# Optimization experiments

Hardware: AMD Instinct MI355X
Metric: run time of the kernel (lower is better)

## Reference

```python
import math
import jax, jax.numpy as jnp
import numpy as np

HIDDEN = 1024
HEADS = 16
HEAD_DIM = HIDDEN // HEADS  # 64
SEQ = 4096
PATCH = 4064  # num rotated (patch) tokens; last PATCH positions get RoPE
EPS = 1e-6


def setup_inputs() -> dict:
    key = jax.random.key(0)
    ks = jax.random.split(key, 8)
    return {
        "x": jax.random.normal(ks[0], (1, SEQ, HIDDEN), dtype=jnp.float32),
        "rope_cos": jax.random.uniform(ks[1], (PATCH, HEAD_DIM // 2), dtype=jnp.float32),
        "rope_sin": jax.random.uniform(ks[2], (PATCH, HEAD_DIM // 2), dtype=jnp.float32),
        "wq": jax.random.normal(ks[3], (HIDDEN, HIDDEN), dtype=jnp.float32) / math.sqrt(HIDDEN),
        "wk": jax.random.normal(ks[4], (HIDDEN, HIDDEN), dtype=jnp.float32) / math.sqrt(HIDDEN),
        "wv": jax.random.normal(ks[5], (HIDDEN, HIDDEN), dtype=jnp.float32) / math.sqrt(HIDDEN),
        "wo": jax.random.normal(ks[6], (HIDDEN, HIDDEN), dtype=jnp.float32) / math.sqrt(HIDDEN),
        "q_norm_w": jnp.ones((HEAD_DIM,), dtype=jnp.float32),
        "k_norm_w": jnp.ones((HEAD_DIM,), dtype=jnp.float32),
    }


def _rms_norm(t, w):
    # RMSNorm over the last (head_dim) axis
    return t * jax.lax.rsqrt(jnp.mean(t * t, axis=-1, keepdims=True) + EPS) * w


def _apply_rope(t, cos, sin):
    # t: [b, s, h, d]; rotate only the last PATCH positions, pairwise complex mul
    b, s, h, d = t.shape
    P = cos.shape[0]
    tail = t[:, s - P:].reshape(b, P, h, d // 2, 2)
    x0, x1 = tail[..., 0], tail[..., 1]
    c = cos[None, :, None, :]
    sn = sin[None, :, None, :]
    rot = jnp.stack([x0 * c - x1 * sn, x0 * sn + x1 * c], axis=-1).reshape(b, P, h, d)
    return jnp.concatenate([t[:, : s - P], rot], axis=1)


def reference(x, rope_cos, rope_sin, wq, wk, wv, wo, q_norm_w, k_norm_w):
    b, s, _ = x.shape
    q = (x @ wq.T).reshape(b, s, HEADS, HEAD_DIM)
    k = (x @ wk.T).reshape(b, s, HEADS, HEAD_DIM)
    v = (x @ wv.T).reshape(b, s, HEADS, HEAD_DIM)
    q = _rms_norm(q, q_norm_w)
    k = _rms_norm(k, k_norm_w)
    q = _apply_rope(q, rope_cos, rope_sin)
    k = _apply_rope(k, rope_cos, rope_sin)
    q = q / math.sqrt(HEAD_DIM)
    scores = jnp.einsum('bqhd,bkhd->bhqk', q, k)
    attn = jax.nn.softmax(scores.astype(jnp.float32), axis=-1)
    out = jnp.einsum('bhqk,bkhd->bqhd', attn, v).reshape(b, s, HIDDEN)
    return out @ wo.T
```

## Files before the change

kernel.cpp:

```cpp
#include <hip/hip_runtime.h>
#include <hip/hip_bf16.h>
#include <stdint.h>

#define HIDDEN 1024
#define HEADS 16
#define HEAD_DIM 64
#define SEQ 4096
#define PATCH 4064
#define SKIP 32

typedef __attribute__((ext_vector_type(8))) short bf16x8;
typedef __attribute__((ext_vector_type(4))) float f32x4;
typedef __attribute__((ext_vector_type(2))) float f32x2;
typedef __attribute__((ext_vector_type(16))) float f32x16;

__device__ __forceinline__ float b2f(unsigned short u){
  union{uint32_t i; float f;} c; c.i = ((uint32_t)u)<<16; return c.f;
}
__device__ __forceinline__ unsigned short f2b(float f){
  union{float f; uint32_t i;} c; c.f=f;
  uint32_t r = c.i + 0x7fffu + ((c.i>>16)&1u);
  return (unsigned short)(r>>16);
}
__device__ __forceinline__ uint32_t cvtpk(float a, float b){
  uint32_t r;
  asm("v_cvt_pk_bf16_f32 %0, %1, %2" : "=v"(r) : "v"(a), "v"(b));
  return r;
}

#define GLD16(gp, lp) __builtin_amdgcn_global_load_lds( \
    (const __attribute__((address_space(1))) void*)(gp), \
    (__attribute__((address_space(3))) void*)(lp), 16, 0, 0)

__global__ __launch_bounds__(256) void convert_all(
    const float* __restrict__ x,  const float* __restrict__ wq,
    const float* __restrict__ wk, const float* __restrict__ wv,
    const float* __restrict__ wo,
    unsigned short* __restrict__ xb,  unsigned short* __restrict__ wqb,
    unsigned short* __restrict__ wkb, unsigned short* __restrict__ wvb,
    unsigned short* __restrict__ wob)
{
  size_t u = (size_t)blockIdx.x*256 + threadIdx.x;
  size_t e = u*8;
  const float* src; unsigned short* dst; size_t off;
  if      (e < 4194304ull) { src=x;  dst=xb;  off=e;            }
  else if (e < 5242880ull) { src=wq; dst=wqb; off=e-4194304ull; }
  else if (e < 6291456ull) { src=wk; dst=wkb; off=e-5242880ull; }
  else if (e < 7340032ull) { src=wv; dst=wvb; off=e-6291456ull; }
  else                     { src=wo; dst=wob; off=e-7340032ull; }
  float4 v0 = *(const float4*)(src+off);
  float4 v1 = *(const float4*)(src+off+4);
  union { bf16x8 v; unsigned short h[8]; } o;
  o.h[0]=f2b(v0.x); o.h[1]=f2b(v0.y); o.h[2]=f2b(v0.z); o.h[3]=f2b(v0.w);
  o.h[4]=f2b(v1.x); o.h[5]=f2b(v1.y); o.h[6]=f2b(v1.z); o.h[7]=f2b(v1.w);
  *(bf16x8*)(dst+off) = o.v;
}

template<int MODE>
__global__ __launch_bounds__(256) void gemm_bt(
    const unsigned short* __restrict__ A,
    const unsigned short* __restrict__ B0,
    const unsigned short* __restrict__ B1,
    const unsigned short* __restrict__ B2,
    float* __restrict__ Cf,
    unsigned short* __restrict__ qout, unsigned short* __restrict__ kout,
    unsigned short* __restrict__ vout,
    const float* __restrict__ rc, const float* __restrict__ rs,
    const float* __restrict__ qw, const float* __restrict__ kw,
    int M, int Nper, int K)
{
  __shared__ unsigned short smem[16384];
  const int tid = threadIdx.x;
  const int w = tid>>6, l = tid&63;
  const int wm = w>>1, wn = w&1;
  const int g = l>>4, lr = l&15;
  const int bm = blockIdx.x;
  int bn = blockIdx.y;
  const int tilesPer = Nper >> 7;
  const int sel = bn / tilesPer;
  bn -= sel*tilesPer;
  const unsigned short* Bsel = (sel==0) ? B0 : ((sel==1) ? B1 : B2);

  const int off0 = w*1024 + l*16;
  const int r0 = off0>>6, c0 = (off0&63)>>1;
  const int off1 = off0 + 4096;
  const int r1 = off1>>6, c1 = (off1&63)>>1;

  const unsigned short* Ab = A    + (size_t)(bm*128)*K;
  const unsigned short* Bb = Bsel + (size_t)(bn*128)*K;

#define STG(db, kt) do { \
    GLD16(Ab + (size_t)r0*K + (kt) + c0, (char*)smem + (db) + off0); \
    GLD16(Ab + (size_t)r1*K + (kt) + c1, (char*)smem + (db) + off1); \
    GLD16(Bb + (size_t)r0*K + (kt) + c0, (char*)smem + (db) + 8192 + off0); \
    GLD16(Bb + (size_t)r1*K + (kt) + c1, (char*)smem + (db) + 8192 + off1); } while(0)

  f32x4 zero = {0.f,0.f,0.f,0.f};
  f32x4 acc[4][4];
  #pragma unroll
  for (int m=0;m<4;m++)
    #pragma unroll
    for (int n=0;n<4;n++) acc[m][n]=zero;

  const int nkt = K >> 5;
  STG(0, 0);
  for (int t = 0; t < nkt; ++t) {
    __syncthreads();
    const int db = (t&1)<<14;
    if (t+1 < nkt) STG(db^16384, (t+1)*32);
    bf16x8 a[4], b[4];
    #pragma unroll
    for (int m=0;m<4;m++)
      a[m] = *(const bf16x8*)((char*)smem + db + (wm*64 + m*16 + lr)*64 + g*16);
    #pragma unroll
    for (int n=0;n<4;n++)
      b[n] = *(const bf16x8*)((char*)smem + db + 8192 + (wn*64 + n*16 + lr)*64 + g*16);
    #pragma unroll
    for (int m=0;m<4;m++)
      #pragma unroll
      for (int n=0;n<4;n++)
        acc[m][n] = __builtin_amdgcn_mfma_f32_16x16x32_bf16(a[m], b[n], acc[m][n], 0,0,0);
  }
#undef STG

  if constexpr (MODE == 0) {
    #pragma unroll
    for (int m=0;m<4;m++){
      const int row = bm*128 + wm*64 + m*16 + g*4;
      #pragma unroll
      for (int n=0;n<4;n++){
        const int col = bn*128 + wn*64 + n*16 + lr;
        #pragma unroll
        for (int r=0;r<4;r++)
          Cf[(size_t)(row+r)*Nper + col] = acc[m][n][r];
      }
    }
  } else {
    if (sel <= 1) {
      const float* nw = (sel==0) ? qw : kw;
      unsigned short* dst = (sel==0) ? qout : kout;
      const float scl = (sel==0) ? 0.18033688011112042f : 1.0f;
      float wl[4];
      #pragma unroll
      for (int n=0;n<4;n++) wl[n] = nw[n*16+lr];
      const int hglob = bn*2 + wn;
      #pragma unroll
      for (int m=0;m<4;m++){
        const int rowb = bm*128 + wm*64 + m*16 + g*4;
        float rn[4];
        #pragma unroll
        for (int r=0;r<4;r++){
          float ss = 0.f;
          #pragma unroll
          for (int n=0;n<4;n++) ss += acc[m][n][r]*acc[m][n][r];
          ss += __shfl_xor(ss,1); ss += __shfl_xor(ss,2);
          ss += __shfl_xor(ss,4); ss += __shfl_xor(ss,8);
          rn[r] = rsqrtf(ss*(1.f/64.f) + 1e-6f);
        }
        #pragma unroll
        for (int r=0;r<4;r++){
          const int row = rowb + r;
          const int p = row - SKIP;
          #pragma unroll
          for (int n=0;n<4;n++){
            float v = acc[m][n][r]*rn[r]*wl[n];
            float c = 1.f, sn = 0.f;
            if (p >= 0){
              const int d2 = (n*16+lr)>>1;
              c  = rc[p*(HEAD_DIM/2) + d2];
              sn = rs[p*(HEAD_DIM/2) + d2];
            }
            const float partner = __shfl_xor(v, 1);
            const float o2 = (lr&1) ? (partner*sn + v*c) : (v*c - partner*sn);
            dst[(size_t)row*HIDDEN + hglob*64 + n*16 + lr] = f2b(o2*scl);
          }
        }
      }
    } else {
      #pragma unroll
      for (int m=0;m<4;m++){
        const int row = bm*128 + wm*64 + m*16 + g*4;
        #pragma unroll
        for (int n=0;n<4;n++){
          const int col = bn*128 + wn*64 + n*16 + lr;
          #pragma unroll
          for (int r=0;r<4;r++)
            vout[(size_t)(row+r)*HIDDEN + col] = f2b(acc[m][n][r]);
        }
      }
    }
  }
}

__global__ __launch_bounds__(256) void transpose_v(
    const unsigned short* __restrict__ v, unsigned short* __restrict__ vt)
{
  __shared__ unsigned short t[64*72];
  const int h = blockIdx.y;
  const int s0 = blockIdx.x * 64;
  const int tid = threadIdx.x;
  #pragma unroll
  for (int i=0;i<2;i++){
    const int e = tid + i*256;
    const int r = e>>3, cc = (e&7)*8;
    *(bf16x8*)&t[r*72+cc] = *(const bf16x8*)(v + (size_t)(s0+r)*HIDDEN + h*HEAD_DIM + cc);
  }
  __syncthreads();
  #pragma unroll
  for (int i=0;i<2;i++){
    const int e = tid + i*256;
    const int d = e>>3, sc = (e&7)*8;
    union { bf16x8 v8; unsigned short h8[8]; } o;
    #pragma unroll
    for (int j=0;j<8;j++){
      const int x  = sc + j;
      const int px = (x & ~12) | ((x&4)<<1) | ((x&8)>>1);
      o.h8[j] = t[px*72 + d];
    }
    *(bf16x8*)(vt + (size_t)(h*HEAD_DIM + d)*SEQ + s0 + sc) = o.v8;
  }
}

__device__ __forceinline__ void softmax_pack(f32x16 (&st)[2], f32x2 &lacc, bf16x8 (&pf)[4]){
  float pv[32];
  #pragma unroll
  for (int i=0;i<16;i++){
    pv[i]    = __builtin_amdgcn_exp2f(st[0][i]);
    pv[16+i] = __builtin_amdgcn_exp2f(st[1][i]);
  }
  #pragma unroll
  for (int i=0;i<8;i++){
    f32x2 a; a.x = pv[2*i];    a.y = pv[2*i+1];    lacc += a;
    f32x2 b; b.x = pv[16+2*i]; b.y = pv[16+2*i+1]; lacc += b;
  }
  #pragma unroll
  for (int t2=0; t2<2; t2++)
    #pragma unroll
    for (int e=0; e<2; e++){
      union { uint32_t u4[4]; bf16x8 v8; } pu;
      #pragma unroll
      for (int u=0; u<4; u++)
        pu.u4[u] = cvtpk(pv[t2*16+e*8+2*u], pv[t2*16+e*8+2*u+1]);
      pf[2*t2+e] = pu.v8;
    }
}

__global__ __launch_bounds__(256, 2) void attn_kernel(
    const unsigned short* __restrict__ q, const unsigned short* __restrict__ k,
    const unsigned short* __restrict__ vt, unsigned short* __restrict__ po,
    float* __restrict__ lbuf)
{
  __shared__ unsigned short smem[32768];
  const int fid = blockIdx.x + 16*(blockIdx.y + 16*blockIdx.z);
  const int h    = (fid&7)*2 + ((fid>>3)&1);
  const int rem  = fid>>4;
  const int q0   = (rem&15)*256;
  const int half = rem>>4;
  const int tid = threadIdx.x;
  const int w = tid>>6, l = tid&63;
  const int hi = l>>5, lo = l&31;
  const int NT = SEQ/128/2;
  const int tbase = half * NT;

  int kcol[4], vcol[4], vrow[4];
  #pragma unroll
  for (int i=0;i<4;i++){
    const int c = tid + i*256;
    const int rk = c>>3;
    kcol[i] = ((c&7)*16) ^ ((rk&7)<<4);
    const int rv = c>>4;
    vrow[i] = rv;
    vcol[i] = (((c&7)*16) ^ ((rv&7)<<4)) + ((c>>3)&1)*128;
  }
  const unsigned short* kPtr[4]; const unsigned short* vPtr[4];
  #pragma unroll
  for (int i=0;i<4;i++){
    kPtr[i] = k  + (size_t)((tid + i*256)>>3)*HIDDEN + h*HEAD_DIM + (kcol[i]>>1);
    vPtr[i] = vt + ((size_t)(h*HEAD_DIM + vrow[i]))*SEQ + (vcol[i]>>1);
  }

#define STAGE(b, kOffE, vOffE) do { \
    GLD16(kPtr[0] + (kOffE), (char*)smem + (b)*32768 + (tid      )*16); \
    GLD16(kPtr[1] + (kOffE), (char*)smem + (b)*32768 + (tid+ 256 )*16); \
    GLD16(kPtr[2] + (kOffE), (char*)smem + (b)*32768 + (tid+ 512 )*16); \
    GLD16(kPtr[3] + (kOffE), (char*)smem + (b)*32768 + (tid+ 768 )*16); \
    GLD16(vPtr[0] + (vOffE), (char*)smem + (b)*32768 + 16384 + (tid      )*16); \
    GLD16(vPtr[1] + (vOffE), (char*)smem + (b)*32768 + 16384 + (tid+ 256 )*16); \
    GLD16(vPtr[2] + (vOffE), (char*)smem + (b)*32768 + 16384 + (tid+ 512 )*16); \
    GLD16(vPtr[3] + (vOffE), (char*)smem + (b)*32768 + 16384 + (tid+ 768 )*16); \
  } while(0)

  const int swz = (lo&7)<<4;
  int colo[4];
  #pragma unroll
  for (int ks=0; ks<4; ks++) colo[ks] = ((2*ks+hi)*16) ^ swz;

  bf16x8 qf0[4], qf1[4];
  {
    const unsigned short* qp = q + (size_t)(q0 + w*64 + lo)*HIDDEN + h*HEAD_DIM;
    #pragma unroll
    for (int ks=0; ks<4; ks++){
      qf0[ks] = *(const bf16x8*)(qp + ks*16 + hi*8);
      qf1[ks] = *(const bf16x8*)(qp + 32*HIDDEN + ks*16 + hi*8);
    }
  }

  f32x16 ot0[2], ot1[2];
  #pragma unroll
  for (int m2=0;m2<2;m2++)
    #pragma unroll
    for (int i=0;i<16;i++){ ot0[m2][i] = 0.f; ot1[m2][i] = 0.f; }
  f32x2 lacc0 = {0.f,0.f}, lacc1 = {0.f,0.f};

  STAGE(0, (size_t)tbase*128*HIDDEN, (size_t)tbase*128);

  for (int t = 0; t < NT; ++t) {
    __syncthreads();
    if (t+1 < NT) {
      const size_t ta = (size_t)(tbase + t + 1);
      STAGE((t+1)&1, ta*128*HIDDEN, ta*128);
    }
    const char* Kb = (const char*)smem + (t&1)*32768;
    const char* Vb = Kb + 16384;

    #pragma unroll
    for (int sub=0; sub<2; ++sub) {
      const char* Ks = Kb + sub*8192;

      f32x16 st0[2], st1[2];
      __builtin_amdgcn_s_setprio(1);
      #pragma unroll
      for (int c=0;c<2;c++){
        #pragma unroll
        for (int i=0;i<16;i++){ st0[c][i] = 0.f; st1[c][i] = 0.f; }
        #pragma unroll
        for (int ks=0; ks<4; ks++){
          bf16x8 a = *(const bf16x8*)(Ks + (32*c+lo)*128 + colo[ks]);
          st0[c] = __builtin_amdgcn_mfma_f32_32x32x16_bf16(a, qf0[ks], st0[c], 0,0,0);
          st1[c] = __builtin_amdgcn_mfma_f32_32x32x16_bf16(a, qf1[ks], st1[c], 0,0,0);
        }
      }
      __builtin_amdgcn_s_setprio(0);

      bf16x8 pf0[4], pf1[4];
      softmax_pack(st0, lacc0, pf0);
      softmax_pack(st1, lacc1, pf1);

      __builtin_amdgcn_s_setprio(1);
      #pragma unroll
      for (int m2=0;m2<2;m2++)
        #pragma unroll
        for (int ks=0; ks<4; ks++){
          bf16x8 a = *(const bf16x8*)(Vb + (32*m2+lo)*256 + sub*128 + colo[ks]);
          ot0[m2] = __builtin_amdgcn_mfma_f32_32x32x16_bf16(a, pf0[ks], ot0[m2], 0,0,0);
          ot1[m2] = __builtin_amdgcn_mfma_f32_32x32x16_bf16(a, pf1[ks], ot1[m2], 0,0,0);
        }
      __builtin_amdgcn_s_setprio(0);
    }
  }

  {
    float ls0 = lacc0.x + lacc0.y;
    ls0 += __shfl_xor(ls0, 32);
    float ls1 = lacc1.x + lacc1.y;
    ls1 += __shfl_xor(ls1, 32);
    if (hi == 0){
      lbuf[(size_t)half*HEADS*SEQ + h*SEQ + q0 + w*64 + lo]      = ls0;
      lbuf[(size_t)half*HEADS*SEQ + h*SEQ + q0 + w*64 + 32 + lo] = ls1;
    }
  }

  __syncthreads();
  #pragma unroll
  for (int m2=0;m2<2;m2++)
    #pragma unroll
    for (int f=0; f<4; f++)
      #pragma unroll
      for (int u=0; u<2; u++){
        const int d = 32*m2 + 8*f + 4*hi + 2*u;
        const uint32_t w0 = cvtpk(ot0[m2][4*f+2*u], ot0[m2][4*f+2*u+1]);
        *(uint32_t*)((char*)smem + (w*64+lo)*128 + ((d*2) ^ swz)) = w0;
        const uint32_t w1 = cvtpk(ot1[m2][4*f+2*u], ot1[m2][4*f+2*u+1]);
        *(uint32_t*)((char*)smem + (w*64+32+lo)*128 + ((d*2) ^ swz)) = w1;
      }
  __syncthreads();
  unsigned short* pout = po + (size_t)half*SEQ*HIDDEN;
  #pragma unroll
  for (int rr=0; rr<2; rr++){
    const int ql = rr*128 + (tid>>1), xh = tid&1;
    #pragma unroll
    for (int i=0;i<4;i++){
      const int cb = xh*64 + i*16;
      bf16x8 vv = *(const bf16x8*)((const char*)smem + ql*128 + (cb ^ ((ql&7)<<4)));
      *(bf16x8*)(pout + (size_t)(q0+ql)*HIDDEN + h*HEAD_DIM + (cb>>1)) = vv;
    }
  }
#undef STAGE
}

__global__ __launch_bounds__(256) void combine_halves(
    const unsigned short* __restrict__ po, const float* __restrict__ lbuf,
    unsigned short* __restrict__ at)
{
  const size_t e = ((size_t)blockIdx.x*256 + threadIdx.x)*8;
  const int qrow = (int)(e >> 10);
  const int h = (int)((e >> 6) & 15);
  const float li = 1.0f / (lbuf[h*SEQ + qrow] + lbuf[HEADS*SEQ + h*SEQ + qrow]);
  union { bf16x8 v; unsigned short s[8]; } a, b, o;
  a.v = *(const bf16x8*)(po + e);
  b.v = *(const bf16x8*)(po + (size_t)SEQ*HIDDEN + e);
  #pragma unroll
  for (int j=0;j<8;j++)
    o.s[j] = f2b((b2f(a.s[j]) + b2f(b.s[j])) * li);
  *(bf16x8*)(at + e) = o.v;
}

extern "C" void kernel_launch(void* const* d_in, const int* in_sizes, int n_in,
                              void* d_out, int out_size, void* d_ws, size_t ws_size,
                              hipStream_t stream)
{
  const float* x  = (const float*)d_in[0];
  const float* rc = (const float*)d_in[1];
  const float* rs = (const float*)d_in[2];
  const float* wq = (const float*)d_in[3];
  const float* wk = (const float*)d_in[4];
  const float* wv = (const float*)d_in[5];
  const float* wo = (const float*)d_in[6];
  const float* qw = (const float*)d_in[7];
  const float* kw = (const float*)d_in[8];
  float* out = (float*)d_out;

  char* ws = (char*)d_ws;
  const size_t MB = 1024*1024;
  unsigned short* xb  = (unsigned short*)(ws + 0);
  unsigned short* wqb = (unsigned short*)(ws + 8*MB);
  unsigned short* wkb = (unsigned short*)(ws + 10*MB);
  unsigned short* wvb = (unsigned short*)(ws + 12*MB);
  unsigned short* wob = (unsigned short*)(ws + 14*MB);
  unsigned short* qkv = (unsigned short*)(ws + 16*MB);
  unsigned short* qb = qkv;
  unsigned short* kb = qkv + (size_t)SEQ*HIDDEN;
  unsigned short* vb = qkv + (size_t)2*SEQ*HIDDEN;
  unsigned short* vt = (unsigned short*)(ws + 0);
  float*          lbuf = (float*)(ws + 8*MB);
  unsigned short* po = (unsigned short*)(ws + 32*MB);
  unsigned short* at = (unsigned short*)(ws + 40*MB);

  convert_all<<<4096, 256, 0, stream>>>(x, wq, wk, wv, wo, xb, wqb, wkb, wvb, wob);
  gemm_bt<1><<<dim3(32,24), 256, 0, stream>>>(
      xb, wqb, wkb, wvb, nullptr, qb, kb, vb, rc, rs, qw, kw,
      SEQ, HIDDEN, HIDDEN);
  transpose_v<<<dim3(64,16), 256, 0, stream>>>(vb, vt);
  attn_kernel<<<dim3(16,16,2), 256, 0, stream>>>(qb, kb, vt, po, lbuf);
  combine_halves<<<2048, 256, 0, stream>>>(po, lbuf, at);
  gemm_bt<0><<<dim3(32,8), 256, 0, stream>>>(
      at, wob, wob, wob, out, nullptr, nullptr, nullptr, nullptr, nullptr, nullptr, nullptr,
      SEQ, HIDDEN, HIDDEN);
}
```

Before: 153.7 us.

## Split output GEMM into narrower tiles and software-pipeline QK across attention sub-tiles

Replaces the templated GEMM with a dedicated QKV kernel and a separate output-projection kernel that uses 128x64 tiles. This doubles the grid from 256 to 512 blocks so the final GEMM fills more of the GPU's compute units. Inside attention, the QK^T products for both 64-key sub-tiles are now computed together before the two softmax/PV phases. That lets the second block of MFMAs overlap the first softmax, at the cost of more accumulator registers (and possibly lower occupancy).

```diff
diff --git a/kernel.cpp b/kernel.cpp
--- a/kernel.cpp
+++ b/kernel.cpp
@@ -56,13 +56,11 @@
   *(bf16x8*)(dst+off) = o.v;
 }
 
-template<int MODE>
-__global__ __launch_bounds__(256) void gemm_bt(
+__global__ __launch_bounds__(256) void gemm_qkv(
     const unsigned short* __restrict__ A,
     const unsigned short* __restrict__ B0,
     const unsigned short* __restrict__ B1,
     const unsigned short* __restrict__ B2,
-    float* __restrict__ Cf,
     unsigned short* __restrict__ qout, unsigned short* __restrict__ kout,
     unsigned short* __restrict__ vout,
     const float* __restrict__ rc, const float* __restrict__ rs,
@@ -123,7 +121,47 @@
   }
 #undef STG
 
-  if constexpr (MODE == 0) {
+  if (sel <= 1) {
+    const float* nw = (sel==0) ? qw : kw;
+    unsigned short* dst = (sel==0) ? qout : kout;
+    const float scl = (sel==0) ? 0.18033688011112042f : 1.0f;
+    float wl[4];
+    #pragma unroll
+    for (int n=0;n<4;n++) wl[n] = nw[n*16+lr];
+    const int hglob = bn*2 + wn;
+    #pragma unroll
+    for (int m=0;m<4;m++){
+      const int rowb = bm*128 + wm*64 + m*16 + g*4;
+      float rn[4];
+      #pragma unroll
+      for (int r=0;r<4;r++){
+        float ss = 0.f;
+        #pragma unroll
+        for (int n=0;n<4;n++) ss += acc[m][n][r]*acc[m][n][r];
+        ss += __shfl_xor(ss,1); ss += __shfl_xor(ss,2);
+        ss += __shfl_xor(ss,4); ss += __shfl_xor(ss,8);
+        rn[r] = rsqrtf(ss*(1.f/64.f) + 1e-6f);
+      }
+      #pragma unroll
+      for (int r=0;r<4;r++){
+        const int row = rowb + r;
+        const int p = row - SKIP;
+        #pragma unroll
+        for (int n=0;n<4;n++){
+          float v = acc[m][n][r]*rn[r]*wl[n];
+          float c = 1.f, sn = 0.f;
+          if (p >= 0){
+            const int d2 = (n*16+lr)>>1;
+            c  = rc[p*(HEAD_DIM/2) + d2];
+            sn = rs[p*(HEAD_DIM/2) + d2];
+          }
+          const float partner = __shfl_xor(v, 1);
+          const float o2 = (lr&1) ? (partner*sn + v*c) : (v*c - partner*sn);
+          dst[(size_t)row*HIDDEN + hglob*64 + n*16 + lr] = f2b(o2*scl);
+        }
+      }
+    }
+  } else {
     #pragma unroll
     for (int m=0;m<4;m++){
       const int row = bm*128 + wm*64 + m*16 + g*4;
@@ -132,62 +170,77 @@
         const int col = bn*128 + wn*64 + n*16 + lr;
         #pragma unroll
         for (int r=0;r<4;r++)
-          Cf[(size_t)(row+r)*Nper + col] = acc[m][n][r];
-      }
-    }
-  } else {
-    if (sel <= 1) {
-      const float* nw = (sel==0) ? qw : kw;
-      unsigned short* dst = (sel==0) ? qout : kout;
-      const float scl = (sel==0) ? 0.18033688011112042f : 1.0f;
-      float wl[4];
-      #pragma unroll
-      for (int n=0;n<4;n++) wl[n] = nw[n*16+lr];
-      const int hglob = bn*2 + wn;
-      #pragma unroll
-      for (int m=0;m<4;m++){
-        const int rowb = bm*128 + wm*64 + m*16 + g*4;
-        float rn[4];
-        #pragma unroll
-        for (int r=0;r<4;r++){
-          float ss = 0.f;
-          #pragma unroll
-          for (int n=0;n<4;n++) ss += acc[m][n][r]*acc[m][n][r];
-          ss += __shfl_xor(ss,1); ss += __shfl_xor(ss,2);
-          ss += __shfl_xor(ss,4); ss += __shfl_xor(ss,8);
-          rn[r] = rsqrtf(ss*(1.f/64.f) + 1e-6f);
-        }
-        #pragma unroll
-        for (int r=0;r<4;r++){
-          const int row = rowb + r;
-          const int p = row - SKIP;
-          #pragma unroll
-          for (int n=0;n<4;n++){
-            float v = acc[m][n][r]*rn[r]*wl[n];
-            float c = 1.f, sn = 0.f;
-            if (p >= 0){
-              const int d2 = (n*16+lr)>>1;
-              c  = rc[p*(HEAD_DIM/2) + d2];
-              sn = rs[p*(HEAD_DIM/2) + d2];
-            }
-            const float partner = __shfl_xor(v, 1);
-            const float o2 = (lr&1) ? (partner*sn + v*c) : (v*c - partner*sn);
-            dst[(size_t)row*HIDDEN + hglob*64 + n*16 + lr] = f2b(o2*scl);
-          }
-        }
-      }
-    } else {
-      #pragma unroll
-      for (int m=0;m<4;m++){
-        const int row = bm*128 + wm*64 + m*16 + g*4;
-        #pragma unroll
-        for (int n=0;n<4;n++){
-          const int col = bn*128 + wn*64 + n*16 + lr;
-          #pragma unroll
-          for (int r=0;r<4;r++)
-            vout[(size_t)(row+r)*HIDDEN + col] = f2b(acc[m][n][r]);
-        }
-      }
+          vout[(size_t)(row+r)*HIDDEN + col] = f2b(acc[m][n][r]);
+      }
+    }
+  }
+}
+
+__global__ __launch_bounds__(256) void gemm_out(
+    const unsigned short* __restrict__ A,
+    const unsigned short* __restrict__ B,
+    float* __restrict__ Cf, int M, int N, int K)
+{
+  __shared__ unsigned short smem[12288];
+  const int tid = threadIdx.x;
+  const int w = tid>>6, l = tid&63;
+  const int wm = w>>1, wn = w&1;
+  const int g = l>>4, lr = l&15;
+  const int bm = blockIdx.x;
+  const int bn = blockIdx.y;
+
+  const int off0 = w*1024 + l*16;
+  const int r0 = off0>>6, c0 = (off0&63)>>1;
+  const int off1 = off0 + 4096;
+  const int r1 = off1>>6, c1 = (off1&63)>>1;
+  const int offB = tid*16;
+  const int rB = offB>>6, cB = (offB&63)>>1;
+
+  const unsigned short* Ab = A + (size_t)(bm*128)*K;
+  const unsigned short* Bb = B + (size_t)(bn*64)*K;
+
+#define STG(db, kt) do { \
+    GLD16(Ab + (size_t)r0*K + (kt) + c0, (char*)smem + (db) + off0); \
+    GLD16(Ab + (size_t)r1*K + (kt) + c1, (char*)smem + (db) + off1); \
+    GLD16(Bb + (size_t)rB*K + (kt) + cB, (char*)smem + (db) + 8192 + offB); } while(0)
+
+  f32x4 zero = {0.f,0.f,0.f,0.f};
+  f32x4 acc[4][2];
+  #pragma unroll
+  for (int m=0;m<4;m++)
+    #pragma unroll
+    for (int n=0;n<2;n++) acc[m][n]=zero;
+
+  const int nkt = K >> 5;
+  STG(0, 0);
+  for (int t = 0; t < nkt; ++t) {
+    __syncthreads();
+    const int db = (t&1)*12288;
+    if (t+1 < nkt) STG(db^12288, (t+1)*32);
+    bf16x8 a[4], b[2];
+    #pragma unroll
+    for (int m=0;m<4;m++)
+      a[m] = *(const bf16x8*)((char*)smem + db + (wm*64 + m*16 + lr)*64 + g*16);
+    #pragma unroll
+    for (int n=0;n<2;n++)
+      b[n] = *(const bf16x8*)((char*)smem + db + 8192 + (wn*32 + n*16 + lr)*64 + g*16);
+    #pragma unroll
+    for (int m=0;m<4;m++)
+      #pragma unroll
+      for (int n=0;n<2;n++)
+        acc[m][n] = __builtin_amdgcn_mfma_f32_16x16x32_bf16(a[m], b[n], acc[m][n], 0,0,0);
+  }
+#undef STG
+
+  #pragma unroll
+  for (int m=0;m<4;m++){
+    const int row = bm*128 + wm*64 + m*16 + g*4;
+    #pragma unroll
+    for (int n=0;n<2;n++){
+      const int col = bn*64 + wn*32 + n*16 + lr;
+      #pragma unroll
+      for (int r=0;r<4;r++)
+        Cf[(size_t)(row+r)*N + col] = acc[m][n][r];
     }
   }
 }
@@ -323,40 +376,56 @@
     const char* Kb = (const char*)smem + (t&1)*32768;
     const char* Vb = Kb + 16384;
 
-    #pragma unroll
-    for (int sub=0; sub<2; ++sub) {
-      const char* Ks = Kb + sub*8192;
-
-      f32x16 st0[2], st1[2];
-      __builtin_amdgcn_s_setprio(1);
-      #pragma unroll
-      for (int c=0;c<2;c++){
-        #pragma unroll
-        for (int i=0;i<16;i++){ st0[c][i] = 0.f; st1[c][i] = 0.f; }
-        #pragma unroll
-        for (int ks=0; ks<4; ks++){
-          bf16x8 a = *(const bf16x8*)(Ks + (32*c+lo)*128 + colo[ks]);
-          st0[c] = __builtin_amdgcn_mfma_f32_32x32x16_bf16(a, qf0[ks], st0[c], 0,0,0);
-          st1[c] = __builtin_amdgcn_mfma_f32_32x32x16_bf16(a, qf1[ks], st1[c], 0,0,0);
-        }
-      }
-      __builtin_amdgcn_s_setprio(0);
-
-      bf16x8 pf0[4], pf1[4];
-      softmax_pack(st0, lacc0, pf0);
-      softmax_pack(st1, lacc1, pf1);
-
-      __builtin_amdgcn_s_setprio(1);
-      #pragma unroll
-      for (int m2=0;m2<2;m2++)
-        #pragma unroll
-        for (int ks=0; ks<4; ks++){
-          bf16x8 a = *(const bf16x8*)(Vb + (32*m2+lo)*256 + sub*128 + colo[ks]);
-          ot0[m2] = __builtin_amdgcn_mfma_f32_32x32x16_bf16(a, pf0[ks], ot0[m2], 0,0,0);
-          ot1[m2] = __builtin_amdgcn_mfma_f32_32x32x16_bf16(a, pf1[ks], ot1[m2], 0,0,0);
-        }
-      __builtin_amdgcn_s_setprio(0);
-    }
+    f32x16 sA0[2], sA1[2], sB0[2], sB1[2];
+    __builtin_amdgcn_s_setprio(1);
+    #pragma unroll
+    for (int c=0;c<2;c++){
+      #pragma unroll
+      for (int i=0;i<16;i++){ sA0[c][i]=0.f; sA1[c][i]=0.f; sB0[c][i]=0.f; sB1[c][i]=0.f; }
+      #pragma unroll
+      for (int ks=0; ks<4; ks++){
+        bf16x8 a0 = *(const bf16x8*)(Kb + (32*c+lo)*128 + colo[ks]);
+        sA0[c] = __builtin_amdgcn_mfma_f32_32x32x16_bf16(a0, qf0[ks], sA0[c], 0,0,0);
+        sA1[c] = __builtin_amdgcn_mfma_f32_32x32x16_bf16(a0, qf1[ks], sA1[c], 0,0,0);
+      }
+      #pragma unroll
+      for (int ks=0; ks<4; ks++){
+        bf16x8 a1 = *(const bf16x8*)(Kb + 8192 + (32*c+lo)*128 + colo[ks]);
+        sB0[c] = __builtin_amdgcn_mfma_f32_32x32x16_bf16(a1, qf0[ks], sB0[c], 0,0,0);
+        sB1[c] = __builtin_amdgcn_mfma_f32_32x32x16_bf16(a1, qf1[ks], sB1[c], 0,0,0);
+      }
+    }
+    __builtin_amdgcn_s_setprio(0);
+
+    bf16x8 pf0[4], pf1[4];
+    softmax_pack(sA0, lacc0, pf0);
+    softmax_pack(sA1, lacc1, pf1);
+
+    __builtin_amdgcn_s_setprio(1);
+    #pragma unroll
+    for (int m2=0;m2<2;m2++)
+      #pragma unroll
+      for (int ks=0; ks<4; ks++){
+        bf16x8 a = *(const bf16x8*)(Vb + (32*m2+lo)*256 + colo[ks]);
+        ot0[m2] = __builtin_amdgcn_mfma_f32_32x32x16_bf16(a, pf0[ks], ot0[m2], 0,0,0);
+        ot1[m2] = __builtin_amdgcn_mfma_f32_32x32x16_bf16(a, pf1[ks], ot1[m2], 0,0,0);
+      }
+    __builtin_amdgcn_s_setprio(0);
+
+    bf16x8 pg0[4], pg1[4];
+    softmax_pack(sB0, lacc0, pg0);
+    softmax_pack(sB1, lacc1, pg1);
+
+    __builtin_amdgcn_s_setprio(1);
+    #pragma unroll
+    for (int m2=0;m2<2;m2++)
+      #pragma unroll
+      for (int ks=0; ks<4; ks++){
+        bf16x8 a = *(const bf16x8*)(Vb + (32*m2+lo)*256 + 128 + colo[ks]);
+        ot0[m2] = __builtin_amdgcn_mfma_f32_32x32x16_bf16(a, pg0[ks], ot0[m2], 0,0,0);
+        ot1[m2] = __builtin_amdgcn_mfma_f32_32x32x16_bf16(a, pg1[ks], ot1[m2], 0,0,0);
+      }
+    __builtin_amdgcn_s_setprio(0);
   }
 
   {
@@ -447,13 +516,10 @@
   unsigned short* at = (unsigned short*)(ws + 40*MB);
 
   convert_all<<<4096, 256, 0, stream>>>(x, wq, wk, wv, wo, xb, wqb, wkb, wvb, wob);
-  gemm_bt<1><<<dim3(32,24), 256, 0, stream>>>(
-      xb, wqb, wkb, wvb, nullptr, qb, kb, vb, rc, rs, qw, kw,
-      SEQ, HIDDEN, HIDDEN);
+  gemm_qkv<<<dim3(32,24), 256, 0, stream>>>(
+      xb, wqb, wkb, wvb, qb, kb, vb, rc, rs, qw, kw, SEQ, HIDDEN, HIDDEN);
   transpose_v<<<dim3(64,16), 256, 0, stream>>>(vb, vt);
   attn_kernel<<<dim3(16,16,2), 256, 0, stream>>>(qb, kb, vt, po, lbuf);
   combine_halves<<<2048, 256, 0, stream>>>(po, lbuf, at);
-  gemm_bt<0><<<dim3(32,8), 256, 0, stream>>>(
-      at, wob, wob, wob, out, nullptr, nullptr, nullptr, nullptr, nullptr, nullptr, nullptr,
-      SEQ, HIDDEN, HIDDEN);
-}
+  gemm_out<<<dim3(32,16), 256, 0, stream>>>(at, wob, out, SEQ, HIDDEN, HIDDEN);
+}
```

New measurement: 174.2 us. 13.4% more time.
